# Performance work log

Measured on AMD Instinct MI355X. Metric: run time of the kernel, lower is better.

## Reference

```python
import jax, jax.numpy as jnp
import numpy as np

B, T, N, IN_DIM, H, C, L, S, P = 64, 13, 325, 2, 64, 4, 2, 4, 12
NC = S * N  # combined temporal-graph node count per batch element


def _make_adj(rng, n, density=0.03):
    mask = rng.random((n, n)) < density
    return (mask * rng.random((n, n))).astype(np.float32)


def _combine(adj, s, forward):
    n = adj.shape[0]
    out = np.zeros((n * s, n * s), np.float32)
    for i in range(s):
        out[i * n:(i + 1) * n, i * n:(i + 1) * n] = adj
        if forward and i < s - 1:
            out[i * n:(i + 1) * n, (i + 1) * n:(i + 2) * n] = np.eye(n, dtype=np.float32)
    return out


def _checkpoints(s, t):
    mark, cp = s, []
    while mark < t:
        cp.append(mark)
        mark += s - 1
    if cp[-1] != t:
        cp.append(t)
    return cp


def setup_inputs():
    key = jax.random.key(0)
    ks = jax.random.split(key, 20)
    rng = np.random.default_rng(0)
    adj = _make_adj(rng, N)
    pea = _make_adj(rng, N)
    sc = 0.05
    inp = {
        'inputs': jax.random.normal(ks[0], (B, T, N, IN_DIM), jnp.float32),
        'adj_fwd': jnp.asarray(_combine(adj, S, True)),
        'adj_bwd': jnp.asarray(_combine(adj, S, False)),
        'pea_fwd': jnp.asarray(_combine(pea, S, True)),
        'pea_bwd': jnp.asarray(_combine(pea, S, False)),
        'w_in': sc * jax.random.normal(ks[1], (IN_DIM, H), jnp.float32),
        'b_in': jnp.zeros((H,), jnp.float32),
        'res_w': sc * jax.random.normal(ks[2], (S,), jnp.float32),
        'res_b': jnp.zeros((), jnp.float32),
        'gconv_w': sc * jax.random.normal(ks[3], (S,), jnp.float32),
        'gconv_b': jnp.zeros((), jnp.float32),
        'gate1_w': sc * jax.random.normal(ks[4], (H, H), jnp.float32),
        'gate1_b': jnp.zeros((H,), jnp.float32),
        'gate2_w': sc * jax.random.normal(ks[5], (H, H * C), jnp.float32),
        'gate2_b': jnp.zeros((H * C,), jnp.float32),
        'reduce_w': sc * jax.random.normal(ks[6], (C * H, H), jnp.float32),
        'reduce_b': jnp.zeros((H,), jnp.float32),
        'gcn_adj_w': sc * jax.random.normal(ks[7], (C, L, 2, H, H), jnp.float32),
        'gcn_adj_b': jnp.zeros((C, L, H), jnp.float32),
        'gcn_pea_w': sc * jax.random.normal(ks[8], (C, L, 2, H, H), jnp.float32),
        'gcn_pea_b': jnp.zeros((C, L, H), jnp.float32),
        'out_conv_w': sc * jax.random.normal(ks[9], (P,), jnp.float32),
        'out_conv_b': jnp.zeros((P,), jnp.float32),
        'out_lin_w': sc * jax.random.normal(ks[10], (H, 1), jnp.float32),
        'out_lin_b': jnp.zeros((1,), jnp.float32),
    }
    return inp


def _gcn_stack(feats, W, b, A_f, A_b, n_out):
    # feats [B, S*N, H]; W [L, 2, H, H]; weighted message passing over both supports
    h = feats
    for l in range(W.shape[0]):
        mf = jnp.einsum('nm,bmh->bnh', A_f, h)
        mb = jnp.einsum('nm,bmh->bnh', A_b, h)
        h = jax.nn.relu(mf @ W[l, 0] + mb @ W[l, 1] + b[l])
    return h[:, -n_out:, :]  # last snapshot's nodes -> [B, N, H]


def reference(inputs, adj_fwd, adj_bwd, pea_fwd, pea_bwd, w_in, b_in, res_w, res_b,
              gconv_w, gconv_b, gate1_w, gate1_b, gate2_w, gate2_b, reduce_w, reduce_b,
              gcn_adj_w, gcn_adj_b, gcn_pea_w, gcn_pea_b, out_conv_w, out_conv_b,
              out_lin_w, out_lin_b):
    b_, t_, n_, _ = inputs.shape
    h_ = w_in.shape[1]
    s_ = res_w.shape[0]
    c_ = gcn_adj_w.shape[0]
    x = inputs @ w_in + b_in  # [B, T, N, H]
    last = None
    left = 0
    for idx, right in enumerate(_checkpoints(s_, t_)):
        fs = x[:, left:right] if idx == 0 else jnp.concatenate([last, x[:, left:right]], axis=1)  # [B,S,N,H]
        gf = (jnp.einsum('s,bsnh->bnh', gconv_w, fs) + gconv_b).reshape(b_ * n_, h_)
        residual = jnp.einsum('s,bsnh->bnh', res_w, fs) + res_b  # [B,N,H]
        feats = fs.reshape(b_, s_ * n_, h_)
        ca = jnp.concatenate(
            [_gcn_stack(feats, gcn_adj_w[c], gcn_adj_b[c], adj_fwd, adj_bwd, n_) for c in range(c_)],
            axis=-1).reshape(b_ * n_, c_ * h_)
        cp = jnp.concatenate(
            [_gcn_stack(feats, gcn_pea_w[c], gcn_pea_b[c], pea_fwd, pea_bwd, n_) for c in range(c_)],
            axis=-1).reshape(b_ * n_, c_ * h_)
        gate = jax.nn.sigmoid(jax.nn.relu(gf @ gate1_w + gate1_b) @ gate2_w + gate2_b)
        gr = gate * ca + (1.0 - gate) * cp
        gr = (gr @ reduce_w + reduce_b).reshape(b_, n_, h_)
        cr = gr + residual
        # nn.LayerNorm([B, N, H], elementwise_affine=False): normalize over whole tensor
        mu = jnp.mean(cr)
        var = jnp.var(cr)
        last = ((cr - mu) * jax.lax.rsqrt(var + 1e-5))[:, None]  # [B,1,N,H]
        left = right
    # 1x1 conv 1->pred_len over channel dim, then linear H->1
    out = jax.nn.relu(out_conv_w.reshape(1, -1, 1, 1) * last + out_conv_b.reshape(1, -1, 1, 1))
    out = out @ out_lin_w + out_lin_b  # [B, pred_len, N, 1]
    return out
```

## Files before the change

### kernel.cpp

```cpp
#include <hip/hip_runtime.h>
#include <hip/hip_bf16.h>
#include <math.h>

#define B_    64
#define T_    13
#define N_    325
#define H_    64
#define C_    4
#define L_    2
#define S_    4
#define P_    12
#define KCP   4
#define M_    (B_*N_)
#define ADJLD 1300
#define NNZCAP 64
#define WPITCH 72
#define MTP   264
#define RTP   264
#define NBLK  1300
#define MIXG  1304

typedef short bfrag __attribute__((ext_vector_type(8)));
typedef float f32x4 __attribute__((ext_vector_type(4)));

__device__ __forceinline__ void fma4(float4& a, float s, float4 x) {
    a.x += s * x.x; a.y += s * x.y; a.z += s * x.z; a.w += s * x.w;
}
__device__ __forceinline__ ushort bf_rne(float f) {
    unsigned u = __float_as_uint(f);
    return (ushort)((u + 0x7fffu + ((u >> 16) & 1u)) >> 16);
}
__device__ __forceinline__ uint2 pack_bf4(float4 v) {
    unsigned a = __float_as_uint(v.x), b = __float_as_uint(v.y);
    unsigned c = __float_as_uint(v.z), d = __float_as_uint(v.w);
    a = (a + 0x7fffu + ((a >> 16) & 1u)) >> 16;
    b = (b + 0x7fffu + ((b >> 16) & 1u)) >> 16;
    c = (c + 0x7fffu + ((c >> 16) & 1u)) >> 16;
    d = (d + 0x7fffu + ((d >> 16) & 1u)) >> 16;
    return make_uint2(a | (b << 16), c | (d << 16));
}
__device__ __forceinline__ float4 unpack_bf4(uint2 p) {
    return make_float4(__uint_as_float(p.x << 16),
                       __uint_as_float(p.x & 0xffff0000u),
                       __uint_as_float(p.y << 16),
                       __uint_as_float(p.y & 0xffff0000u));
}

__global__ void k_setup(
    const float* __restrict__ adj_fwd, const float* __restrict__ pea_fwd,
    const float* __restrict__ gadj_w, const float* __restrict__ gpea_w,
    const float* __restrict__ reduce_w,
    const float* __restrict__ gate1_w, const float* __restrict__ gate2_w,
    int* __restrict__ cnt, int* __restrict__ cols, float* __restrict__ vals,
    ushort* __restrict__ WT,
    ushort* __restrict__ RT, ushort* __restrict__ W1T, ushort* __restrict__ W2T)
{
    int bid = blockIdx.x, t = threadIdx.x;
    if (bid < 163) {
        int lane = t & 63, w = t >> 6;
        int row = bid * 4 + w;
        if (row >= 2 * N_) return;
        int mat = (row >= N_) ? 1 : 0;
        int n   = row - mat * N_;
        const float* A = mat ? pea_fwd : adj_fwd;
        const float* rp = A + (size_t)n * ADJLD;
        int* cw   = cols + (size_t)row * NNZCAP;
        float* vw = vals + (size_t)row * NNZCAP;
        int c = 0;
        for (int c0 = 0; c0 < 384; c0 += 64) {
            int col = c0 + lane;
            float v = (col < N_) ? rp[col] : 0.f;
            unsigned long long mmask = __ballot(v != 0.f);
            int idx = c + __popcll(mmask & ((1ull << lane) - 1ull));
            if (v != 0.f && idx < NNZCAP) { cw[idx] = col; vw[idx] = v; }
            c += __popcll(mmask);
        }
        if (c + lane < NNZCAP) { cw[c + lane] = 0; vw[c + lane] = 0.f; }
        if (lane == 0) cnt[row] = (c < NNZCAP) ? c : NNZCAP;
    } else if (bid == 163) {
        for (int i = 0; i < 64; ++i) {
            int e = t + i * 256;
            int k = e >> 6, n = e & 63;
            RT[(size_t)n * RTP + k] = bf_rne(reduce_w[e]);
        }
    } else if (bid < 180) {
        int mat = bid - 164;
        int layer = mat >> 3, sm = mat & 7;
        int stack = sm >> 2, c = sm & 3;
        const float* w0 = (stack ? gpea_w : gadj_w) + (size_t)((c * L_ + layer) * 2) * 4096;
        const float* w1 = w0 + 4096;
        for (int i = 0; i < 16; ++i) {
            int e = t + i * 256;
            int k = e >> 6, n = e & 63;
            WT[((size_t)mat * 64 + n) * WPITCH + k] = bf_rne(w0[e] + w1[e]);
        }
    } else if (bid == 180) {
        for (int i = 0; i < 16; ++i) {
            int e = t + i * 256;
            int k = e >> 6, n = e & 63;
            W1T[(size_t)n * WPITCH + k] = bf_rne(gate1_w[e]);
        }
    } else {
        for (int i = 0; i < 64; ++i) {
            int e = t + i * 256;
            int k = e >> 8, n = e & 255;
            W2T[(size_t)n * WPITCH + k] = bf_rne(gate2_w[e]);
        }
    }
}

__device__ __forceinline__ void l1_block(
    int vb, int t, int tt,
    const int*   __restrict__ cnt,
    const int*   __restrict__ cols,
    const float* __restrict__ vals,
    const float* __restrict__ inp,
    const float* __restrict__ w_in, const float* __restrict__ b_in,
    const ushort* __restrict__ WT,
    const float* __restrict__ badj, const float* __restrict__ bpea,
    ushort* __restrict__ G1a, ushort* __restrict__ G1p,
    ushort* MaH, ushort* MpH)
{
    int lane = t & 63, w = t >> 6;
    int m0 = vb * 32;
    int q = lane >> 4, ml = lane & 15;
    int colg = w * 16 + ml;

    bfrag BF[8][2];
    #pragma unroll
    for (int mat = 0; mat < 8; ++mat)
        #pragma unroll
        for (int kc = 0; kc < 2; ++kc)
            BF[mat][kc] = *(const bfrag*)&WT[((size_t)mat * 64 + colg) * WPITCH + kc * 32 + q * 8];

    {
        int row_l  = lane & 7;
        int stackl = (lane >> 3) & 1;
        int part   = lane >> 4;
        int m = m0 + w * 8 + row_l;
        int b = m / N_;
        int n = m - b * N_;
        const float* ipb = inp + ((size_t)(b * T_ + tt) * N_) * 2;
        int rowidx = stackl * N_ + n;
        const int*   cp = cols + (size_t)rowidx * NNZCAP;
        const float* vp = vals + (size_t)rowidx * NNZCAP;
        int myc = cnt[rowidx];
        float s0 = 0.f, s1 = 0.f, sv = 0.f;
        int   cn = cp[part];
        float vn = vp[part];
        for (int j = part; j < myc; j += 4) {
            int   c = cn;
            float v = vn;
            cn = cp[j + 4];
            vn = vp[j + 4];
            float2 x = *(const float2*)&ipb[(size_t)c * 2];
            s0 += v * x.x; s1 += v * x.y; sv += v;
        }
        s0 += __shfl_xor(s0, 16); s1 += __shfl_xor(s1, 16); sv += __shfl_xor(sv, 16);
        s0 += __shfl_xor(s0, 32); s1 += __shfl_xor(s1, 32); sv += __shfl_xor(sv, 32);
        float wa = w_in[lane], wb = w_in[H_ + lane], bi = b_in[lane];
        #pragma unroll
        for (int r = 0; r < 8; ++r) {
            float a0 = __shfl(s0, r),     a1 = __shfl(s1, r),     av = __shfl(sv, r);
            float p0 = __shfl(s0, 8 + r), p1 = __shfl(s1, 8 + r), pv = __shfl(sv, 8 + r);
            MaH[(w * 8 + r) * WPITCH + lane] = bf_rne(a0 * wa + a1 * wb + av * bi);
            MpH[(w * 8 + r) * WPITCH + lane] = bf_rne(p0 * wa + p1 * wb + pv * bi);
        }
    }
    __syncthreads();

    #pragma unroll
    for (int sc = 0; sc < 8; ++sc) {
        int stack = sc >> 2, c = sc & 3;
        const ushort* Msrc = stack ? MpH : MaH;
        float bv = (stack ? bpea : badj)[c * L_ * H_ + colg];
        ushort* Gout = stack ? G1p : G1a;
        #pragma unroll
        for (int r = 0; r < 2; ++r) {
            bfrag A0 = *(const bfrag*)&Msrc[(16 * r + ml) * WPITCH + q * 8];
            bfrag A1 = *(const bfrag*)&Msrc[(16 * r + ml) * WPITCH + 32 + q * 8];
            f32x4 acc = {0.f, 0.f, 0.f, 0.f};
            acc = __builtin_amdgcn_mfma_f32_16x16x32_bf16(A0, BF[sc][0], acc, 0, 0, 0);
            acc = __builtin_amdgcn_mfma_f32_16x16x32_bf16(A1, BF[sc][1], acc, 0, 0, 0);
            #pragma unroll
            for (int j = 0; j < 4; ++j) {
                float v = acc[j] + bv;
                v = v > 0.f ? v : 0.f;
                Gout[(size_t)(m0 + 16 * r + q * 4 + j) * 256 + c * 64 + colg] = bf_rne(v);
            }
        }
    }
}

__global__ __launch_bounds__(256, 4) void k_layer1(
    const int*   __restrict__ cnt,
    const int*   __restrict__ cols,
    const float* __restrict__ vals,
    const float* __restrict__ inp,
    const float* __restrict__ w_in, const float* __restrict__ b_in,
    const ushort* __restrict__ WT,
    const float* __restrict__ badj, const float* __restrict__ bpea,
    ushort* __restrict__ G1a4, ushort* __restrict__ G1p4)
{
    __shared__ __align__(16) ushort MaH[32 * WPITCH];
    __shared__ __align__(16) ushort MpH[32 * WPITCH];
    int vb = (blockIdx.x & 7) * 82 + (blockIdx.x >> 3);
    if (vb >= 650) return;
    l1_block(vb, threadIdx.x, 3, cnt, cols, vals,
             inp, w_in, b_in, WT, badj, bpea, G1a4, G1p4, MaH, MpH);
}

__global__ __launch_bounds__(256, 4) void k_mix(
    const float* __restrict__ inp,
    const float* __restrict__ w_in, const float* __restrict__ b_in,
    const float* __restrict__ gconv_w, const float* __restrict__ gconv_b,
    const float* __restrict__ res_w,   const float* __restrict__ res_b,
    const float* __restrict__ cr_in, int it,
    const ushort* __restrict__ W1T, const float* __restrict__ b1,
    const ushort* __restrict__ W2T, const float* __restrict__ b2,
    const int*   __restrict__ cnt,
    const int*   __restrict__ cols,
    const float* __restrict__ vals,
    const ushort* __restrict__ G1a, const ushort* __restrict__ G1p,
    const ushort* __restrict__ WT,
    const float* __restrict__ badj, const float* __restrict__ bpea,
    const ushort* __restrict__ RT,
    const float* __restrict__ reduce_b,
    float* __restrict__ cr,
    const float* __restrict__ partials_in,
    float* __restrict__ partials,
    int tt_l1,
    ushort* __restrict__ G1a_wr, ushort* __restrict__ G1p_wr)
{
    __shared__ __align__(16) ushort MtA[16 * MTP];
    __shared__ __align__(16) ushort MtP[16 * MTP];
    __shared__ __align__(16) ushort Gf[16 * WPITCH];
    __shared__ __align__(16) ushort Gr[16 * WPITCH];
    __shared__ float RES[16 * 68];
    __shared__ float red[8];
    int t = threadIdx.x, lane = t & 63, w = t >> 6;

    if (blockIdx.x >= MIXG) {
        int lx = blockIdx.x - MIXG;
        int vb1 = (lx & 7) * 82 + (lx >> 3);
        if (vb1 >= 650) return;
        l1_block(vb1, t, tt_l1, cnt, cols, vals, inp, w_in, b_in,
                 WT, badj, bpea, G1a_wr, G1p_wr, (ushort*)MtA, (ushort*)MtP);
        return;
    }

    int vb = (blockIdx.x & 7) * 163 + (blockIdx.x >> 3);
    if (vb >= NBLK) return;
    int m0 = vb * 16;
    int q = lane >> 4, ml = lane & 15;
    int colg = w * 16 + ml;

    float mu = 0.f, rs = 0.f;
    if (it > 0) {
        float a = 0.f, b = 0.f;
        for (int i = t; i < NBLK; i += 256) { a += partials_in[i]; b += partials_in[NBLK + i]; }
        #pragma unroll
        for (int off = 32; off > 0; off >>= 1) {
            a += __shfl_xor(a, off);
            b += __shfl_xor(b, off);
        }
        if (lane == 0) { red[w] = a; red[4 + w] = b; }
        __syncthreads();
        a = red[0] + red[1] + red[2] + red[3];
        b = red[4] + red[5] + red[6] + red[7];
        const float inv = 1.f / (float)(M_ * H_);
        mu = a * inv;
        float var = b * inv - mu * mu;
        rs = rsqrtf(var + 1e-5f);
    }

    {
        float wa = w_in[lane], wb = w_in[H_ + lane], bi = b_in[lane];
        float gw0 = gconv_w[0], gw1 = gconv_w[1], gw2 = gconv_w[2], gw3 = gconv_w[3];
        float rw0 = res_w[0],   rw1 = res_w[1],   rw2 = res_w[2],   rw3 = res_w[3];
        float gb = gconv_b[0],  rb = res_b[0];
        int t1 = (it == 0) ? 1 : (3 * it + 1);
        for (int i = 0; i < 4; ++i) {
            int r = i * 4 + w;
            int m = m0 + r;
            int b = m / N_, n = m % N_;
            const float* ipb = inp + ((size_t)b * T_ * N_ + n) * 2;
            float v0;
            if (it > 0) v0 = (cr_in[(size_t)m * H_ + lane] - mu) * rs;
            else        v0 = ipb[0] * wa + ipb[1] * wb + bi;
            const float* ip1 = ipb + (size_t)t1 * N_ * 2;
            const float* ip2 = ip1 + (size_t)N_ * 2;
            const float* ip3 = ip2 + (size_t)N_ * 2;
            float v1 = ip1[0] * wa + ip1[1] * wb + bi;
            float v2 = ip2[0] * wa + ip2[1] * wb + bi;
            float v3 = ip3[0] * wa + ip3[1] * wb + bi;
            Gf[r * WPITCH + lane] = bf_rne(gb + gw0 * v0 + gw1 * v1 + gw2 * v2 + gw3 * v3);
            RES[r * 68 + lane]    = rb + rw0 * v0 + rw1 * v1 + rw2 * v2 + rw3 * v3;
        }
    }
    __syncthreads();

    {
        bfrag A0 = *(const bfrag*)&Gf[ml * WPITCH + q * 8];
        bfrag A1 = *(const bfrag*)&Gf[ml * WPITCH + 32 + q * 8];
        bfrag B0 = *(const bfrag*)&W1T[(size_t)colg * WPITCH + q * 8];
        bfrag B1 = *(const bfrag*)&W1T[(size_t)colg * WPITCH + 32 + q * 8];
        f32x4 acc = {0.f, 0.f, 0.f, 0.f};
        acc = __builtin_amdgcn_mfma_f32_16x16x32_bf16(A0, B0, acc, 0, 0, 0);
        acc = __builtin_amdgcn_mfma_f32_16x16x32_bf16(A1, B1, acc, 0, 0, 0);
        float bb = b1[colg];
        #pragma unroll
        for (int j = 0; j < 4; ++j) {
            float v = acc[j] + bb;
            v = v > 0.f ? v : 0.f;
            Gr[(q * 4 + j) * WPITCH + colg] = bf_rne(v);
        }
    }
    __syncthreads();

    f32x4 gsv[4];
    {
        bfrag A0 = *(const bfrag*)&Gr[ml * WPITCH + q * 8];
        bfrag A1 = *(const bfrag*)&Gr[ml * WPITCH + 32 + q * 8];
        #pragma unroll
        for (int c = 0; c < 4; ++c) {
            bfrag B0 = *(const bfrag*)&W2T[(size_t)(c * 64 + colg) * WPITCH + q * 8];
            bfrag B1 = *(const bfrag*)&W2T[(size_t)(c * 64 + colg) * WPITCH + 32 + q * 8];
            f32x4 acc = {0.f, 0.f, 0.f, 0.f};
            acc = __builtin_amdgcn_mfma_f32_16x16x32_bf16(A0, B0, acc, 0, 0, 0);
            acc = __builtin_amdgcn_mfma_f32_16x16x32_bf16(A1, B1, acc, 0, 0, 0);
            float bb = b2[c * 64 + colg];
            #pragma unroll
            for (int j = 0; j < 4; ++j)
                gsv[c][j] = 1.f / (1.f + expf(-(acc[j] + bb)));
        }
    }

    for (int pp = 0; pp < 4; pp += 2) {
        int ma = m0 + w * 4 + pp, mb = ma + 1;
        int na = ma % N_, nb = mb % N_;
        const ushort* ga = G1a + (size_t)(ma - na) * 256 + lane * 4;
        const ushort* gb = G1a + (size_t)(mb - nb) * 256 + lane * 4;
        const ushort* pa = G1p + (size_t)(ma - na) * 256 + lane * 4;
        const ushort* pb = G1p + (size_t)(mb - nb) * 256 + lane * 4;
        const int   *cA0 = cols + na * NNZCAP,        *cB0 = cols + nb * NNZCAP;
        const float *vA0 = vals + na * NNZCAP,        *vB0 = vals + nb * NNZCAP;
        const int   *cA1 = cols + (N_ + na) * NNZCAP, *cB1 = cols + (N_ + nb) * NNZCAP;
        const float *vA1 = vals + (N_ + na) * NNZCAP, *vB1 = vals + (N_ + nb) * NNZCAP;
        int jm = max(max(cnt[na], cnt[nb]), max(cnt[N_ + na], cnt[N_ + nb]));
        float4 a0 = make_float4(0.f,0.f,0.f,0.f), a1 = make_float4(0.f,0.f,0.f,0.f);
        float4 p0 = make_float4(0.f,0.f,0.f,0.f), p1 = make_float4(0.f,0.f,0.f,0.f);
        int   nA00 = cA0[0], nA01 = cA0[1], nB00 = cB0[0], nB01 = cB0[1];
        int   nA10 = cA1[0], nA11 = cA1[1], nB10 = cB1[0], nB11 = cB1[1];
        float mA00 = vA0[0], mA01 = vA0[1], mB00 = vB0[0], mB01 = vB0[1];
        float mA10 = vA1[0], mA11 = vA1[1], mB10 = vB1[0], mB11 = vB1[1];
        for (int j = 0; j < jm; j += 2) {
            int   iA00 = nA00, iA01 = nA01, iB00 = nB00, iB01 = nB01;
            int   iA10 = nA10, iA11 = nA11, iB10 = nB10, iB11 = nB11;
            float uA00 = mA00, uA01 = mA01, uB00 = mB00, uB01 = mB01;
            float uA10 = mA10, uA11 = mA11, uB10 = mB10, uB11 = mB11;
            nA00 = cA0[j+2]; nA01 = cA0[j+3]; nB00 = cB0[j+2]; nB01 = cB0[j+3];
            nA10 = cA1[j+2]; nA11 = cA1[j+3]; nB10 = cB1[j+2]; nB11 = cB1[j+3];
            mA00 = vA0[j+2]; mA01 = vA0[j+3]; mB00 = vB0[j+2]; mB01 = vB0[j+3];
            mA10 = vA1[j+2]; mA11 = vA1[j+3]; mB10 = vB1[j+2]; mB11 = vB1[j+3];
            fma4(a0, uA00, unpack_bf4(*(const uint2*)&ga[iA00 * 256]));
            fma4(a0, uA01, unpack_bf4(*(const uint2*)&ga[iA01 * 256]));
            fma4(a1, uB00, unpack_bf4(*(const uint2*)&gb[iB00 * 256]));
            fma4(a1, uB01, unpack_bf4(*(const uint2*)&gb[iB01 * 256]));
            fma4(p0, uA10, unpack_bf4(*(const uint2*)&pa[iA10 * 256]));
            fma4(p0, uA11, unpack_bf4(*(const uint2*)&pa[iA11 * 256]));
            fma4(p1, uB10, unpack_bf4(*(const uint2*)&pb[iB10 * 256]));
            fma4(p1, uB11, unpack_bf4(*(const uint2*)&pb[iB11 * 256]));
        }
        int row0 = w * 4 + pp;
        *(uint2*)&MtA[row0 * MTP + lane * 4]       = pack_bf4(a0);
        *(uint2*)&MtA[(row0 + 1) * MTP + lane * 4] = pack_bf4(a1);
        *(uint2*)&MtP[row0 * MTP + lane * 4]       = pack_bf4(p0);
        *(uint2*)&MtP[(row0 + 1) * MTP + lane * 4] = pack_bf4(p1);
    }
    __syncthreads();

    const ushort* WT1 = WT + (size_t)8 * 64 * WPITCH;
    f32x4 res[4];
    bfrag B0c = *(const bfrag*)&WT1[(size_t)colg * WPITCH + q * 8];
    bfrag B1c = *(const bfrag*)&WT1[(size_t)colg * WPITCH + 32 + q * 8];
    #pragma unroll
    for (int sc = 0; sc < 8; ++sc) {
        int stack = sc >> 2, c = sc & 3;
        bfrag B0n = B0c, B1n = B1c;
        if (sc < 7) {
            B0n = *(const bfrag*)&WT1[((size_t)(sc + 1) * 64 + colg) * WPITCH + q * 8];
            B1n = *(const bfrag*)&WT1[((size_t)(sc + 1) * 64 + colg) * WPITCH + 32 + q * 8];
        }
        const ushort* Msrc = stack ? MtP : MtA;
        float bv = (stack ? bpea : badj)[(c * L_ + 1) * H_ + colg];
        bfrag A0 = *(const bfrag*)&Msrc[ml * MTP + c * 64 + q * 8];
        bfrag A1 = *(const bfrag*)&Msrc[ml * MTP + c * 64 + 32 + q * 8];
        f32x4 acc = {0.f, 0.f, 0.f, 0.f};
        acc = __builtin_amdgcn_mfma_f32_16x16x32_bf16(A0, B0c, acc, 0, 0, 0);
        acc = __builtin_amdgcn_mfma_f32_16x16x32_bf16(A1, B1c, acc, 0, 0, 0);
        #pragma unroll
        for (int j = 0; j < 4; ++j) {
            float v = acc[j] + bv;
            v = v > 0.f ? v : 0.f;
            if (stack == 0) res[c][j] = gsv[c][j] * v;
            else            res[c][j] += (1.f - gsv[c][j]) * v;
        }
        B0c = B0n; B1c = B1n;
    }

    bfrag RF[8];
    #pragma unroll
    for (int kc = 0; kc < 8; ++kc)
        RF[kc] = *(const bfrag*)&RT[(size_t)colg * RTP + kc * 32 + q * 8];
    f32x4 rv;
    #pragma unroll
    for (int j = 0; j < 4; ++j)
        rv[j] = RES[(q * 4 + j) * 68 + colg];

    __syncthreads();
    #pragma unroll
    for (int c = 0; c < 4; ++c)
        #pragma unroll
        for (int j = 0; j < 4; ++j)
            MtA[(q * 4 + j) * MTP + c * 64 + colg] = bf_rne(res[c][j]);
    __syncthreads();

    f32x4 racc = {0.f, 0.f, 0.f, 0.f};
    #pragma unroll
    for (int kc = 0; kc < 8; ++kc) {
        bfrag A0 = *(const bfrag*)&MtA[ml * MTP + kc * 32 + q * 8];
        racc = __builtin_amdgcn_mfma_f32_16x16x32_bf16(A0, RF[kc], racc, 0, 0, 0);
    }

    float bi = reduce_b[colg];
    float s = 0.f, s2 = 0.f;
    #pragma unroll
    for (int j = 0; j < 4; ++j) {
        int m = m0 + q * 4 + j;
        float v = racc[j] + bi + rv[j];
        cr[(size_t)m * 64 + colg] = v;
        s += v; s2 += v * v;
    }
    #pragma unroll
    for (int off = 32; off > 0; off >>= 1) {
        s  += __shfl_xor(s, off);
        s2 += __shfl_xor(s2, off);
    }
    if (lane == 0) { red[w] = s; red[4 + w] = s2; }
    __syncthreads();
    if (t == 0) partials[vb]        = red[0] + red[1] + red[2] + red[3];
    if (t == 1) partials[NBLK + vb] = red[4] + red[5] + red[6] + red[7];
}

__global__ __launch_bounds__(64) void k_out(
    const float* __restrict__ cr, const float* __restrict__ partials,
    const float* __restrict__ ocw, const float* __restrict__ ocb,
    const float* __restrict__ olw, const float* __restrict__ olb,
    float* __restrict__ out) {
    int t = threadIdx.x;
    float a = 0.f, b2s = 0.f;
    for (int i = t; i < NBLK; i += 64) { a += partials[i]; b2s += partials[NBLK + i]; }
    #pragma unroll
    for (int off = 32; off > 0; off >>= 1) {
        a   += __shfl_xor(a, off);
        b2s += __shfl_xor(b2s, off);
    }
    const float inv = 1.f / (float)(M_ * H_);
    float mu  = a * inv;
    float var = b2s * inv - mu * mu;
    float rs  = rsqrtf(var + 1e-5f);

    int m = blockIdx.x * 64 + t;
    int b = m / N_, n = m % N_;
    float cw[P_], cb[P_], acc[P_];
    #pragma unroll
    for (int p = 0; p < P_; ++p) { cw[p] = ocw[p]; cb[p] = ocb[p]; acc[p] = 0.f; }
    const float* lr = cr + (size_t)m * H_;
    for (int h4 = 0; h4 < 64; h4 += 4) {
        float4 lv4 = *(const float4*)&lr[h4];
        float4 wv4 = *(const float4*)&olw[h4];
        float lv[4] = {(lv4.x - mu) * rs, (lv4.y - mu) * rs,
                       (lv4.z - mu) * rs, (lv4.w - mu) * rs};
        float wv[4] = {wv4.x, wv4.y, wv4.z, wv4.w};
        #pragma unroll
        for (int e = 0; e < 4; ++e) {
            float lvv = lv[e], wvv = wv[e];
            #pragma unroll
            for (int p = 0; p < P_; ++p) {
                float u = cw[p] * lvv + cb[p];
                u = u > 0.f ? u : 0.f;
                acc[p] += u * wvv;
            }
        }
    }
    float ob = olb[0];
    #pragma unroll
    for (int p = 0; p < P_; ++p)
        out[(size_t)(b * P_ + p) * N_ + n] = acc[p] + ob;
}

extern "C" void kernel_launch(void* const* d_in, const int* in_sizes, int n_in,
                              void* d_out, int out_size, void* d_ws, size_t ws_size,
                              hipStream_t stream) {
    const float* inp      = (const float*)d_in[0];
    const float* adj_fwd  = (const float*)d_in[1];
    const float* pea_fwd  = (const float*)d_in[3];
    const float* w_in     = (const float*)d_in[5];
    const float* b_in     = (const float*)d_in[6];
    const float* res_w    = (const float*)d_in[7];
    const float* res_b    = (const float*)d_in[8];
    const float* gconv_w  = (const float*)d_in[9];
    const float* gconv_b  = (const float*)d_in[10];
    const float* gate1_w  = (const float*)d_in[11];
    const float* gate1_b  = (const float*)d_in[12];
    const float* gate2_w  = (const float*)d_in[13];
    const float* gate2_b  = (const float*)d_in[14];
    const float* reduce_w = (const float*)d_in[15];
    const float* reduce_b = (const float*)d_in[16];
    const float* gadj_w   = (const float*)d_in[17];
    const float* gadj_b   = (const float*)d_in[18];
    const float* gpea_w   = (const float*)d_in[19];
    const float* gpea_b   = (const float*)d_in[20];
    const float* ocw      = (const float*)d_in[21];
    const float* ocb      = (const float*)d_in[22];
    const float* olw      = (const float*)d_in[23];
    const float* olb      = (const float*)d_in[24];
    float* out = (float*)d_out;

    float* ws       = (float*)d_ws;
    float* cr       = ws;
    float* partials = cr + (size_t)M_ * H_;
    int*   scnt  = (int*)(partials + 2 * NBLK);
    int*   scols = scnt + 2 * N_;
    float* svals = (float*)(scols + 2 * N_ * NNZCAP);
    ushort* G1a4 = (ushort*)(svals + 2 * N_ * NNZCAP);
    ushort* G1p4 = G1a4 + 2 * (size_t)M_ * 256;
    ushort* WT   = G1p4 + 2 * (size_t)M_ * 256;
    WT = (ushort*)(((uintptr_t)WT + 15) & ~(uintptr_t)15);
    ushort* RT   = WT + 16 * 64 * WPITCH;
    ushort* W1T  = RT + 64 * RTP;
    ushort* W2T  = W1T + 64 * WPITCH;

    k_setup<<<182, 256, 0, stream>>>(
        adj_fwd, pea_fwd, gadj_w, gpea_w, reduce_w,
        gate1_w, gate2_w, scnt, scols, svals, WT, RT, W1T, W2T);

    k_layer1<<<656, 256, 0, stream>>>(
        scnt, scols, svals, inp, w_in, b_in, WT, gadj_b, gpea_b, G1a4, G1p4);

    for (int it = 0; it < 4; ++it) {
        int slot = it & 1;
        int embed = (it < 3);
        int grid  = MIXG + (embed ? 656 : 0);
        int wrsl  = (it + 1) & 1;
        k_mix<<<grid, 256, 0, stream>>>(
            inp, w_in, b_in, gconv_w, gconv_b, res_w, res_b, cr, it,
            W1T, gate1_b, W2T, gate2_b,
            scnt, scols, svals,
            G1a4 + (size_t)slot * M_ * 256, G1p4 + (size_t)slot * M_ * 256,
            WT, gadj_b, gpea_b, RT, reduce_b, cr, partials, partials,
            3 * (it + 1) + 3,
            G1a4 + (size_t)wrsl * M_ * 256, G1p4 + (size_t)wrsl * M_ * 256);
    }

    k_out<<<N_, 64, 0, stream>>>(cr, partials, ocw, ocb, olw, olb, out);
}
```

Before: 402.1 us.

## Fuse all stages into one cooperative persistent kernel with grid syncs

Replaces the chain of setup, layer-1, four mix launches and output launch with a single cooperative kernel that loops over the stages persistently and separates them with grid-wide barriers. Partial statistics are double-buffered so one stage's LayerNorm partials are not overwritten while they are still being read. The aim is to remove kernel launch gaps and tail effects between the roughly seven dependent launches. The cost is grid.sync overhead and a grid capped by occupancy, so blocks loop over the work. The original multi-launch path is kept as a fallback if the cooperative launch fails.

```diff
diff --git a/kernel.cpp b/kernel.cpp
--- a/kernel.cpp
+++ b/kernel.cpp
@@ -1,6 +1,9 @@
 #include <hip/hip_runtime.h>
 #include <hip/hip_bf16.h>
+#include <hip/hip_cooperative_groups.h>
 #include <math.h>
+
+namespace cg = cooperative_groups;
 
 #define B_    64
 #define T_    13
@@ -10,7 +13,6 @@
 #define L_    2
 #define S_    4
 #define P_    12
-#define KCP   4
 #define M_    (B_*N_)
 #define ADJLD 1300
 #define NNZCAP 64
@@ -46,26 +48,29 @@
                        __uint_as_float(p.y & 0xffff0000u));
 }
 
-__global__ void k_setup(
-    const float* __restrict__ adj_fwd, const float* __restrict__ pea_fwd,
-    const float* __restrict__ gadj_w, const float* __restrict__ gpea_w,
-    const float* __restrict__ reduce_w,
-    const float* __restrict__ gate1_w, const float* __restrict__ gate2_w,
-    int* __restrict__ cnt, int* __restrict__ cols, float* __restrict__ vals,
-    ushort* __restrict__ WT,
-    ushort* __restrict__ RT, ushort* __restrict__ W1T, ushort* __restrict__ W2T)
-{
-    int bid = blockIdx.x, t = threadIdx.x;
+struct MP {
+    const float *inp, *adj_fwd, *pea_fwd;
+    const float *w_in, *b_in, *res_w, *res_b, *gconv_w, *gconv_b;
+    const float *gate1_w, *gate1_b, *gate2_w, *gate2_b;
+    const float *reduce_w, *reduce_b;
+    const float *gadj_w, *gadj_b, *gpea_w, *gpea_b;
+    const float *ocw, *ocb, *olw, *olb;
+    int *scnt; int *scols; float *svals;
+    ushort *G1a4, *G1p4, *WT, *RT, *W1T, *W2T;
+    float *cr, *pb0, *pb1, *out;
+};
+
+__device__ __forceinline__ void do_setup(int bid, int t, const MP& p) {
     if (bid < 163) {
         int lane = t & 63, w = t >> 6;
         int row = bid * 4 + w;
         if (row >= 2 * N_) return;
         int mat = (row >= N_) ? 1 : 0;
         int n   = row - mat * N_;
-        const float* A = mat ? pea_fwd : adj_fwd;
+        const float* A = mat ? p.pea_fwd : p.adj_fwd;
         const float* rp = A + (size_t)n * ADJLD;
-        int* cw   = cols + (size_t)row * NNZCAP;
-        float* vw = vals + (size_t)row * NNZCAP;
+        int* cw   = p.scols + (size_t)row * NNZCAP;
+        float* vw = p.svals + (size_t)row * NNZCAP;
         int c = 0;
         for (int c0 = 0; c0 < 384; c0 += 64) {
             int col = c0 + lane;
@@ -76,48 +81,41 @@
             c += __popcll(mmask);
         }
         if (c + lane < NNZCAP) { cw[c + lane] = 0; vw[c + lane] = 0.f; }
-        if (lane == 0) cnt[row] = (c < NNZCAP) ? c : NNZCAP;
+        if (lane == 0) p.scnt[row] = (c < NNZCAP) ? c : NNZCAP;
     } else if (bid == 163) {
         for (int i = 0; i < 64; ++i) {
             int e = t + i * 256;
             int k = e >> 6, n = e & 63;
-            RT[(size_t)n * RTP + k] = bf_rne(reduce_w[e]);
+            p.RT[(size_t)n * RTP + k] = bf_rne(p.reduce_w[e]);
         }
     } else if (bid < 180) {
         int mat = bid - 164;
         int layer = mat >> 3, sm = mat & 7;
         int stack = sm >> 2, c = sm & 3;
-        const float* w0 = (stack ? gpea_w : gadj_w) + (size_t)((c * L_ + layer) * 2) * 4096;
+        const float* w0 = (stack ? p.gpea_w : p.gadj_w) + (size_t)((c * L_ + layer) * 2) * 4096;
         const float* w1 = w0 + 4096;
         for (int i = 0; i < 16; ++i) {
             int e = t + i * 256;
             int k = e >> 6, n = e & 63;
-            WT[((size_t)mat * 64 + n) * WPITCH + k] = bf_rne(w0[e] + w1[e]);
+            p.WT[((size_t)mat * 64 + n) * WPITCH + k] = bf_rne(w0[e] + w1[e]);
         }
     } else if (bid == 180) {
         for (int i = 0; i < 16; ++i) {
             int e = t + i * 256;
             int k = e >> 6, n = e & 63;
-            W1T[(size_t)n * WPITCH + k] = bf_rne(gate1_w[e]);
-        }
-    } else {
+            p.W1T[(size_t)n * WPITCH + k] = bf_rne(p.gate1_w[e]);
+        }
+    } else if (bid == 181) {
         for (int i = 0; i < 64; ++i) {
             int e = t + i * 256;
             int k = e >> 8, n = e & 255;
-            W2T[(size_t)n * WPITCH + k] = bf_rne(gate2_w[e]);
+            p.W2T[(size_t)n * WPITCH + k] = bf_rne(p.gate2_w[e]);
         }
     }
 }
 
 __device__ __forceinline__ void l1_block(
-    int vb, int t, int tt,
-    const int*   __restrict__ cnt,
-    const int*   __restrict__ cols,
-    const float* __restrict__ vals,
-    const float* __restrict__ inp,
-    const float* __restrict__ w_in, const float* __restrict__ b_in,
-    const ushort* __restrict__ WT,
-    const float* __restrict__ badj, const float* __restrict__ bpea,
+    int vb, int t, int tt, const MP& p,
     ushort* __restrict__ G1a, ushort* __restrict__ G1p,
     ushort* MaH, ushort* MpH)
 {
@@ -131,7 +129,7 @@
     for (int mat = 0; mat < 8; ++mat)
         #pragma unroll
         for (int kc = 0; kc < 2; ++kc)
-            BF[mat][kc] = *(const bfrag*)&WT[((size_t)mat * 64 + colg) * WPITCH + kc * 32 + q * 8];
+            BF[mat][kc] = *(const bfrag*)&p.WT[((size_t)mat * 64 + colg) * WPITCH + kc * 32 + q * 8];
 
     {
         int row_l  = lane & 7;
@@ -140,11 +138,11 @@
         int m = m0 + w * 8 + row_l;
         int b = m / N_;
         int n = m - b * N_;
-        const float* ipb = inp + ((size_t)(b * T_ + tt) * N_) * 2;
+        const float* ipb = p.inp + ((size_t)(b * T_ + tt) * N_) * 2;
         int rowidx = stackl * N_ + n;
-        const int*   cp = cols + (size_t)rowidx * NNZCAP;
-        const float* vp = vals + (size_t)rowidx * NNZCAP;
-        int myc = cnt[rowidx];
+        const int*   cp = p.scols + (size_t)rowidx * NNZCAP;
+        const float* vp = p.svals + (size_t)rowidx * NNZCAP;
+        int myc = p.scnt[rowidx];
         float s0 = 0.f, s1 = 0.f, sv = 0.f;
         int   cn = cp[part];
         float vn = vp[part];
@@ -158,7 +156,7 @@
         }
         s0 += __shfl_xor(s0, 16); s1 += __shfl_xor(s1, 16); sv += __shfl_xor(sv, 16);
         s0 += __shfl_xor(s0, 32); s1 += __shfl_xor(s1, 32); sv += __shfl_xor(sv, 32);
-        float wa = w_in[lane], wb = w_in[H_ + lane], bi = b_in[lane];
+        float wa = p.w_in[lane], wb = p.w_in[H_ + lane], bi = p.b_in[lane];
         #pragma unroll
         for (int r = 0; r < 8; ++r) {
             float a0 = __shfl(s0, r),     a1 = __shfl(s1, r),     av = __shfl(sv, r);
@@ -173,7 +171,7 @@
     for (int sc = 0; sc < 8; ++sc) {
         int stack = sc >> 2, c = sc & 3;
         const ushort* Msrc = stack ? MpH : MaH;
-        float bv = (stack ? bpea : badj)[c * L_ * H_ + colg];
+        float bv = (stack ? p.gpea_b : p.gadj_b)[c * L_ * H_ + colg];
         ushort* Gout = stack ? G1p : G1a;
         #pragma unroll
         for (int r = 0; r < 2; ++r) {
@@ -192,65 +190,13 @@
     }
 }
 
-__global__ __launch_bounds__(256, 4) void k_layer1(
-    const int*   __restrict__ cnt,
-    const int*   __restrict__ cols,
-    const float* __restrict__ vals,
-    const float* __restrict__ inp,
-    const float* __restrict__ w_in, const float* __restrict__ b_in,
-    const ushort* __restrict__ WT,
-    const float* __restrict__ badj, const float* __restrict__ bpea,
-    ushort* __restrict__ G1a4, ushort* __restrict__ G1p4)
+__device__ __forceinline__ void mix_block(
+    int vb, int t, int it, const MP& p,
+    const ushort* __restrict__ G1a, const ushort* __restrict__ G1p,
+    const float* __restrict__ pin, float* __restrict__ pout,
+    ushort* MtA, ushort* MtP, ushort* Gf, ushort* Gr, float* RES, float* red)
 {
-    __shared__ __align__(16) ushort MaH[32 * WPITCH];
-    __shared__ __align__(16) ushort MpH[32 * WPITCH];
-    int vb = (blockIdx.x & 7) * 82 + (blockIdx.x >> 3);
-    if (vb >= 650) return;
-    l1_block(vb, threadIdx.x, 3, cnt, cols, vals,
-             inp, w_in, b_in, WT, badj, bpea, G1a4, G1p4, MaH, MpH);
-}
-
-__global__ __launch_bounds__(256, 4) void k_mix(
-    const float* __restrict__ inp,
-    const float* __restrict__ w_in, const float* __restrict__ b_in,
-    const float* __restrict__ gconv_w, const float* __restrict__ gconv_b,
-    const float* __restrict__ res_w,   const float* __restrict__ res_b,
-    const float* __restrict__ cr_in, int it,
-    const ushort* __restrict__ W1T, const float* __restrict__ b1,
-    const ushort* __restrict__ W2T, const float* __restrict__ b2,
-    const int*   __restrict__ cnt,
-    const int*   __restrict__ cols,
-    const float* __restrict__ vals,
-    const ushort* __restrict__ G1a, const ushort* __restrict__ G1p,
-    const ushort* __restrict__ WT,
-    const float* __restrict__ badj, const float* __restrict__ bpea,
-    const ushort* __restrict__ RT,
-    const float* __restrict__ reduce_b,
-    float* __restrict__ cr,
-    const float* __restrict__ partials_in,
-    float* __restrict__ partials,
-    int tt_l1,
-    ushort* __restrict__ G1a_wr, ushort* __restrict__ G1p_wr)
-{
-    __shared__ __align__(16) ushort MtA[16 * MTP];
-    __shared__ __align__(16) ushort MtP[16 * MTP];
-    __shared__ __align__(16) ushort Gf[16 * WPITCH];
-    __shared__ __align__(16) ushort Gr[16 * WPITCH];
-    __shared__ float RES[16 * 68];
-    __shared__ float red[8];
-    int t = threadIdx.x, lane = t & 63, w = t >> 6;
-
-    if (blockIdx.x >= MIXG) {
-        int lx = blockIdx.x - MIXG;
-        int vb1 = (lx & 7) * 82 + (lx >> 3);
-        if (vb1 >= 650) return;
-        l1_block(vb1, t, tt_l1, cnt, cols, vals, inp, w_in, b_in,
-                 WT, badj, bpea, G1a_wr, G1p_wr, (ushort*)MtA, (ushort*)MtP);
-        return;
-    }
-
-    int vb = (blockIdx.x & 7) * 163 + (blockIdx.x >> 3);
-    if (vb >= NBLK) return;
+    int lane = t & 63, w = t >> 6;
     int m0 = vb * 16;
     int q = lane >> 4, ml = lane & 15;
     int colg = w * 16 + ml;
@@ -258,7 +204,7 @@
     float mu = 0.f, rs = 0.f;
     if (it > 0) {
         float a = 0.f, b = 0.f;
-        for (int i = t; i < NBLK; i += 256) { a += partials_in[i]; b += partials_in[NBLK + i]; }
+        for (int i = t; i < NBLK; i += 256) { a += pin[i]; b += pin[NBLK + i]; }
         #pragma unroll
         for (int off = 32; off > 0; off >>= 1) {
             a += __shfl_xor(a, off);
@@ -275,18 +221,18 @@
     }
 
     {
-        float wa = w_in[lane], wb = w_in[H_ + lane], bi = b_in[lane];
-        float gw0 = gconv_w[0], gw1 = gconv_w[1], gw2 = gconv_w[2], gw3 = gconv_w[3];
-        float rw0 = res_w[0],   rw1 = res_w[1],   rw2 = res_w[2],   rw3 = res_w[3];
-        float gb = gconv_b[0],  rb = res_b[0];
+        float wa = p.w_in[lane], wb = p.w_in[H_ + lane], bi = p.b_in[lane];
+        float gw0 = p.gconv_w[0], gw1 = p.gconv_w[1], gw2 = p.gconv_w[2], gw3 = p.gconv_w[3];
+        float rw0 = p.res_w[0],   rw1 = p.res_w[1],   rw2 = p.res_w[2],   rw3 = p.res_w[3];
+        float gb = p.gconv_b[0],  rb = p.res_b[0];
         int t1 = (it == 0) ? 1 : (3 * it + 1);
         for (int i = 0; i < 4; ++i) {
             int r = i * 4 + w;
             int m = m0 + r;
             int b = m / N_, n = m % N_;
-            const float* ipb = inp + ((size_t)b * T_ * N_ + n) * 2;
+            const float* ipb = p.inp + ((size_t)b * T_ * N_ + n) * 2;
             float v0;
-            if (it > 0) v0 = (cr_in[(size_t)m * H_ + lane] - mu) * rs;
+            if (it > 0) v0 = (p.cr[(size_t)m * H_ + lane] - mu) * rs;
             else        v0 = ipb[0] * wa + ipb[1] * wb + bi;
             const float* ip1 = ipb + (size_t)t1 * N_ * 2;
             const float* ip2 = ip1 + (size_t)N_ * 2;
@@ -303,12 +249,12 @@
     {
         bfrag A0 = *(const bfrag*)&Gf[ml * WPITCH + q * 8];
         bfrag A1 = *(const bfrag*)&Gf[ml * WPITCH + 32 + q * 8];
-        bfrag B0 = *(const bfrag*)&W1T[(size_t)colg * WPITCH + q * 8];
-        bfrag B1 = *(const bfrag*)&W1T[(size_t)colg * WPITCH + 32 + q * 8];
+        bfrag B0 = *(const bfrag*)&p.W1T[(size_t)colg * WPITCH + q * 8];
+        bfrag B1 = *(const bfrag*)&p.W1T[(size_t)colg * WPITCH + 32 + q * 8];
         f32x4 acc = {0.f, 0.f, 0.f, 0.f};
         acc = __builtin_amdgcn_mfma_f32_16x16x32_bf16(A0, B0, acc, 0, 0, 0);
         acc = __builtin_amdgcn_mfma_f32_16x16x32_bf16(A1, B1, acc, 0, 0, 0);
-        float bb = b1[colg];
+        float bb = p.gate1_b[colg];
         #pragma unroll
         for (int j = 0; j < 4; ++j) {
             float v = acc[j] + bb;
@@ -324,12 +270,12 @@
         bfrag A1 = *(const bfrag*)&Gr[ml * WPITCH + 32 + q * 8];
         #pragma unroll
         for (int c = 0; c < 4; ++c) {
-            bfrag B0 = *(const bfrag*)&W2T[(size_t)(c * 64 + colg) * WPITCH + q * 8];
-            bfrag B1 = *(const bfrag*)&W2T[(size_t)(c * 64 + colg) * WPITCH + 32 + q * 8];
+            bfrag B0 = *(const bfrag*)&p.W2T[(size_t)(c * 64 + colg) * WPITCH + q * 8];
+            bfrag B1 = *(const bfrag*)&p.W2T[(size_t)(c * 64 + colg) * WPITCH + 32 + q * 8];
             f32x4 acc = {0.f, 0.f, 0.f, 0.f};
             acc = __builtin_amdgcn_mfma_f32_16x16x32_bf16(A0, B0, acc, 0, 0, 0);
             acc = __builtin_amdgcn_mfma_f32_16x16x32_bf16(A1, B1, acc, 0, 0, 0);
-            float bb = b2[c * 64 + colg];
+            float bb = p.gate2_b[c * 64 + colg];
             #pragma unroll
             for (int j = 0; j < 4; ++j)
                 gsv[c][j] = 1.f / (1.f + expf(-(acc[j] + bb)));
@@ -343,11 +289,11 @@
         const ushort* gb = G1a + (size_t)(mb - nb) * 256 + lane * 4;
         const ushort* pa = G1p + (size_t)(ma - na) * 256 + lane * 4;
         const ushort* pb = G1p + (size_t)(mb - nb) * 256 + lane * 4;
-        const int   *cA0 = cols + na * NNZCAP,        *cB0 = cols + nb * NNZCAP;
-        const float *vA0 = vals + na * NNZCAP,        *vB0 = vals + nb * NNZCAP;
-        const int   *cA1 = cols + (N_ + na) * NNZCAP, *cB1 = cols + (N_ + nb) * NNZCAP;
-        const float *vA1 = vals + (N_ + na) * NNZCAP, *vB1 = vals + (N_ + nb) * NNZCAP;
-        int jm = max(max(cnt[na], cnt[nb]), max(cnt[N_ + na], cnt[N_ + nb]));
+        const int   *cA0 = p.scols + na * NNZCAP,        *cB0 = p.scols + nb * NNZCAP;
+        const float *vA0 = p.svals + na * NNZCAP,        *vB0 = p.svals + nb * NNZCAP;
+        const int   *cA1 = p.scols + (N_ + na) * NNZCAP, *cB1 = p.scols + (N_ + nb) * NNZCAP;
+        const float *vA1 = p.svals + (N_ + na) * NNZCAP, *vB1 = p.svals + (N_ + nb) * NNZCAP;
+        int jm = max(max(p.scnt[na], p.scnt[nb]), max(p.scnt[N_ + na], p.scnt[N_ + nb]));
         float4 a0 = make_float4(0.f,0.f,0.f,0.f), a1 = make_float4(0.f,0.f,0.f,0.f);
         float4 p0 = make_float4(0.f,0.f,0.f,0.f), p1 = make_float4(0.f,0.f,0.f,0.f);
         int   nA00 = cA0[0], nA01 = cA0[1], nB00 = cB0[0], nB01 = cB0[1];
@@ -380,7 +326,7 @@
     }
     __syncthreads();
 
-    const ushort* WT1 = WT + (size_t)8 * 64 * WPITCH;
+    const ushort* WT1 = p.WT + (size_t)8 * 64 * WPITCH;
     f32x4 res[4];
     bfrag B0c = *(const bfrag*)&WT1[(size_t)colg * WPITCH + q * 8];
     bfrag B1c = *(const bfrag*)&WT1[(size_t)colg * WPITCH + 32 + q * 8];
@@ -393,7 +339,7 @@
             B1n = *(const bfrag*)&WT1[((size_t)(sc + 1) * 64 + colg) * WPITCH + 32 + q * 8];
         }
         const ushort* Msrc = stack ? MtP : MtA;
-        float bv = (stack ? bpea : badj)[(c * L_ + 1) * H_ + colg];
+        float bv = (stack ? p.gpea_b : p.gadj_b)[(c * L_ + 1) * H_ + colg];
         bfrag A0 = *(const bfrag*)&Msrc[ml * MTP + c * 64 + q * 8];
         bfrag A1 = *(const bfrag*)&Msrc[ml * MTP + c * 64 + 32 + q * 8];
         f32x4 acc = {0.f, 0.f, 0.f, 0.f};
@@ -412,7 +358,7 @@
     bfrag RF[8];
     #pragma unroll
     for (int kc = 0; kc < 8; ++kc)
-        RF[kc] = *(const bfrag*)&RT[(size_t)colg * RTP + kc * 32 + q * 8];
+        RF[kc] = *(const bfrag*)&p.RT[(size_t)colg * RTP + kc * 32 + q * 8];
     f32x4 rv;
     #pragma unroll
     for (int j = 0; j < 4; ++j)
@@ -433,13 +379,13 @@
         racc = __builtin_amdgcn_mfma_f32_16x16x32_bf16(A0, RF[kc], racc, 0, 0, 0);
     }
 
-    float bi = reduce_b[colg];
+    float bi = p.reduce_b[colg];
     float s = 0.f, s2 = 0.f;
     #pragma unroll
     for (int j = 0; j < 4; ++j) {
         int m = m0 + q * 4 + j;
         float v = racc[j] + bi + rv[j];
-        cr[(size_t)m * 64 + colg] = v;
+        p.cr[(size_t)m * 64 + colg] = v;
         s += v; s2 += v * v;
     }
     #pragma unroll
@@ -449,37 +395,170 @@
     }
     if (lane == 0) { red[w] = s; red[4 + w] = s2; }
     __syncthreads();
-    if (t == 0) partials[vb]        = red[0] + red[1] + red[2] + red[3];
-    if (t == 1) partials[NBLK + vb] = red[4] + red[5] + red[6] + red[7];
-}
-
-__global__ __launch_bounds__(64) void k_out(
-    const float* __restrict__ cr, const float* __restrict__ partials,
-    const float* __restrict__ ocw, const float* __restrict__ ocb,
-    const float* __restrict__ olw, const float* __restrict__ olb,
-    float* __restrict__ out) {
-    int t = threadIdx.x;
+    if (t == 0) pout[vb]        = red[0] + red[1] + red[2] + red[3];
+    if (t == 1) pout[NBLK + vb] = red[4] + red[5] + red[6] + red[7];
+}
+
+__device__ __forceinline__ void do_out(int bid, int t, const MP& p,
+                                       const float* __restrict__ pbuf, float* red)
+{
+    int lane = t & 63, w = t >> 6;
     float a = 0.f, b2s = 0.f;
-    for (int i = t; i < NBLK; i += 64) { a += partials[i]; b2s += partials[NBLK + i]; }
+    for (int i = t; i < NBLK; i += 256) { a += pbuf[i]; b2s += pbuf[NBLK + i]; }
     #pragma unroll
     for (int off = 32; off > 0; off >>= 1) {
         a   += __shfl_xor(a, off);
         b2s += __shfl_xor(b2s, off);
     }
+    if (lane == 0) { red[w] = a; red[4 + w] = b2s; }
+    __syncthreads();
+    a   = red[0] + red[1] + red[2] + red[3];
+    b2s = red[4] + red[5] + red[6] + red[7];
     const float inv = 1.f / (float)(M_ * H_);
     float mu  = a * inv;
     float var = b2s * inv - mu * mu;
     float rs  = rsqrtf(var + 1e-5f);
 
+    int m = bid * 256 + t;
+    if (m >= M_) return;
+    int b = m / N_, n = m % N_;
+    float cw[P_], cb[P_], acc[P_];
+    #pragma unroll
+    for (int pp = 0; pp < P_; ++pp) { cw[pp] = p.ocw[pp]; cb[pp] = p.ocb[pp]; acc[pp] = 0.f; }
+    const float* lr = p.cr + (size_t)m * H_;
+    for (int h4 = 0; h4 < 64; h4 += 4) {
+        float4 lv4 = *(const float4*)&lr[h4];
+        float4 wv4 = *(const float4*)&p.olw[h4];
+        float lv[4] = {(lv4.x - mu) * rs, (lv4.y - mu) * rs,
+                       (lv4.z - mu) * rs, (lv4.w - mu) * rs};
+        float wv[4] = {wv4.x, wv4.y, wv4.z, wv4.w};
+        #pragma unroll
+        for (int e = 0; e < 4; ++e) {
+            float lvv = lv[e], wvv = wv[e];
+            #pragma unroll
+            for (int pp = 0; pp < P_; ++pp) {
+                float u = cw[pp] * lvv + cb[pp];
+                u = u > 0.f ? u : 0.f;
+                acc[pp] += u * wvv;
+            }
+        }
+    }
+    float ob = p.olb[0];
+    #pragma unroll
+    for (int pp = 0; pp < P_; ++pp)
+        p.out[(size_t)(b * P_ + pp) * N_ + n] = acc[pp] + ob;
+}
+
+__global__ __launch_bounds__(256, 4) void k_mega(MP p)
+{
+    __shared__ __align__(16) ushort MtA[16 * MTP];
+    __shared__ __align__(16) ushort MtP[16 * MTP];
+    __shared__ __align__(16) ushort Gf[16 * WPITCH];
+    __shared__ __align__(16) ushort Gr[16 * WPITCH];
+    __shared__ float RES[16 * 68];
+    __shared__ float red[8];
+    cg::grid_group grid = cg::this_grid();
+    int bid = blockIdx.x, t = threadIdx.x, G = gridDim.x;
+
+    if (bid < 182) do_setup(bid, t, p);
+    grid.sync();
+
+    for (int v = bid; v < 656; v += G) {
+        int vb = (v & 7) * 82 + (v >> 3);
+        if (vb < 650)
+            l1_block(vb, t, 3, p, p.G1a4, p.G1p4, (ushort*)MtA, (ushort*)MtP);
+        __syncthreads();
+    }
+    grid.sync();
+
+    for (int it = 0; it < 4; ++it) {
+        const float* pin  = (it & 1) ? p.pb0 : p.pb1;
+        float*       pout = (it & 1) ? p.pb1 : p.pb0;
+        const ushort* G1a_rd = p.G1a4 + (size_t)(it & 1) * M_ * 256;
+        const ushort* G1p_rd = p.G1p4 + (size_t)(it & 1) * M_ * 256;
+        ushort* G1a_wr = p.G1a4 + (size_t)((it + 1) & 1) * M_ * 256;
+        ushort* G1p_wr = p.G1p4 + (size_t)((it + 1) & 1) * M_ * 256;
+        int nv  = (it < 3) ? (MIXG + 656) : MIXG;
+        int tt1 = 3 * (it + 1) + 3;
+        for (int v = bid; v < nv; v += G) {
+            if (v < MIXG) {
+                int vb = (v & 7) * 163 + (v >> 3);
+                if (vb < NBLK)
+                    mix_block(vb, t, it, p, G1a_rd, G1p_rd, pin, pout,
+                              MtA, MtP, Gf, Gr, RES, red);
+            } else {
+                int lx = v - MIXG;
+                int vb1 = (lx & 7) * 82 + (lx >> 3);
+                if (vb1 < 650)
+                    l1_block(vb1, t, tt1, p, G1a_wr, G1p_wr, (ushort*)MtA, (ushort*)MtP);
+            }
+            __syncthreads();
+        }
+        grid.sync();
+    }
+
+    if (bid * 256 < M_) do_out(bid, t, p, p.pb1, red);
+}
+
+__global__ void k_setup(MP p) { do_setup(blockIdx.x, threadIdx.x, p); }
+
+__global__ __launch_bounds__(256, 4) void k_layer1(MP p) {
+    __shared__ __align__(16) ushort MaH[32 * WPITCH];
+    __shared__ __align__(16) ushort MpH[32 * WPITCH];
+    int vb = (blockIdx.x & 7) * 82 + (blockIdx.x >> 3);
+    if (vb >= 650) return;
+    l1_block(vb, threadIdx.x, 3, p, p.G1a4, p.G1p4, MaH, MpH);
+}
+
+__global__ __launch_bounds__(256, 4) void k_mix(MP p, int it) {
+    __shared__ __align__(16) ushort MtA[16 * MTP];
+    __shared__ __align__(16) ushort MtP[16 * MTP];
+    __shared__ __align__(16) ushort Gf[16 * WPITCH];
+    __shared__ __align__(16) ushort Gr[16 * WPITCH];
+    __shared__ float RES[16 * 68];
+    __shared__ float red[8];
+    int t = threadIdx.x;
+    if (blockIdx.x >= MIXG) {
+        int lx = blockIdx.x - MIXG;
+        int vb1 = (lx & 7) * 82 + (lx >> 3);
+        if (vb1 >= 650) return;
+        l1_block(vb1, t, 3 * (it + 1) + 3, p,
+                 p.G1a4 + (size_t)((it + 1) & 1) * M_ * 256,
+                 p.G1p4 + (size_t)((it + 1) & 1) * M_ * 256,
+                 (ushort*)MtA, (ushort*)MtP);
+        return;
+    }
+    int vb = (blockIdx.x & 7) * 163 + (blockIdx.x >> 3);
+    if (vb >= NBLK) return;
+    mix_block(vb, t, it, p,
+              p.G1a4 + (size_t)(it & 1) * M_ * 256,
+              p.G1p4 + (size_t)(it & 1) * M_ * 256,
+              p.pb0, p.pb0, MtA, MtP, Gf, Gr, RES, red);
+}
+
+__global__ __launch_bounds__(64) void k_out(MP p) {
+    int t = threadIdx.x;
+    float a = 0.f, b2s = 0.f;
+    for (int i = t; i < NBLK; i += 64) { a += p.pb0[i]; b2s += p.pb0[NBLK + i]; }
+    #pragma unroll
+    for (int off = 32; off > 0; off >>= 1) {
+        a   += __shfl_xor(a, off);
+        b2s += __shfl_xor(b2s, off);
+    }
+    const float inv = 1.f / (float)(M_ * H_);
+    float mu  = a * inv;
+    float var = b2s * inv - mu * mu;
+    float rs  = rsqrtf(var + 1e-5f);
+
     int m = blockIdx.x * 64 + t;
     int b = m / N_, n = m % N_;
     float cw[P_], cb[P_], acc[P_];
     #pragma unroll
-    for (int p = 0; p < P_; ++p) { cw[p] = ocw[p]; cb[p] = ocb[p]; acc[p] = 0.f; }
-    const float* lr = cr + (size_t)m * H_;
+    for (int pp = 0; pp < P_; ++pp) { cw[pp] = p.ocw[pp]; cb[pp] = p.ocb[pp]; acc[pp] = 0.f; }
+    const float* lr = p.cr + (size_t)m * H_;
     for (int h4 = 0; h4 < 64; h4 += 4) {
         float4 lv4 = *(const float4*)&lr[h4];
-        float4 wv4 = *(const float4*)&olw[h4];
+        float4 wv4 = *(const float4*)&p.olw[h4];
         float lv[4] = {(lv4.x - mu) * rs, (lv4.y - mu) * rs,
                        (lv4.z - mu) * rs, (lv4.w - mu) * rs};
         float wv[4] = {wv4.x, wv4.y, wv4.z, wv4.w};
@@ -487,82 +566,80 @@
         for (int e = 0; e < 4; ++e) {
             float lvv = lv[e], wvv = wv[e];
             #pragma unroll
-            for (int p = 0; p < P_; ++p) {
-                float u = cw[p] * lvv + cb[p];
+            for (int pp = 0; pp < P_; ++pp) {
+                float u = cw[pp] * lvv + cb[pp];
                 u = u > 0.f ? u : 0.f;
-                acc[p] += u * wvv;
+                acc[pp] += u * wvv;
             }
         }
     }
-    float ob = olb[0];
-    #pragma unroll
-    for (int p = 0; p < P_; ++p)
-        out[(size_t)(b * P_ + p) * N_ + n] = acc[p] + ob;
+    float ob = p.olb[0];
+    #pragma unroll
+    for (int pp = 0; pp < P_; ++pp)
+        p.out[(size_t)(b * P_ + pp) * N_ + n] = acc[pp] + ob;
 }
 
 extern "C" void kernel_launch(void* const* d_in, const int* in_sizes, int n_in,
                               void* d_out, int out_size, void* d_ws, size_t ws_size,
                               hipStream_t stream) {
-    const float* inp      = (const float*)d_in[0];
-    const float* adj_fwd  = (const float*)d_in[1];
-    const float* pea_fwd  = (const float*)d_in[3];
-    const float* w_in     = (const float*)d_in[5];
-    const float* b_in     = (const float*)d_in[6];
-    const float* res_w    = (const float*)d_in[7];
-    const float* res_b    = (const float*)d_in[8];
-    const float* gconv_w  = (const float*)d_in[9];
-    const float* gconv_b  = (const float*)d_in[10];
-    const float* gate1_w  = (const float*)d_in[11];
-    const float* gate1_b  = (const float*)d_in[12];
-    const float* gate2_w  = (const float*)d_in[13];
-    const float* gate2_b  = (const float*)d_in[14];
-    const float* reduce_w = (const float*)d_in[15];
-    const float* reduce_b = (const float*)d_in[16];
-    const float* gadj_w   = (const float*)d_in[17];
-    const float* gadj_b   = (const float*)d_in[18];
-    const float* gpea_w   = (const float*)d_in[19];
-    const float* gpea_b   = (const float*)d_in[20];
-    const float* ocw      = (const float*)d_in[21];
-    const float* ocb      = (const float*)d_in[22];
-    const float* olw      = (const float*)d_in[23];
-    const float* olb      = (const float*)d_in[24];
-    float* out = (float*)d_out;
-
-    float* ws       = (float*)d_ws;
-    float* cr       = ws;
-    float* partials = cr + (size_t)M_ * H_;
-    int*   scnt  = (int*)(partials + 2 * NBLK);
-    int*   scols = scnt + 2 * N_;
-    float* svals = (float*)(scols + 2 * N_ * NNZCAP);
-    ushort* G1a4 = (ushort*)(svals + 2 * N_ * NNZCAP);
-    ushort* G1p4 = G1a4 + 2 * (size_t)M_ * 256;
-    ushort* WT   = G1p4 + 2 * (size_t)M_ * 256;
+    MP p;
+    p.inp      = (const float*)d_in[0];
+    p.adj_fwd  = (const float*)d_in[1];
+    p.pea_fwd  = (const float*)d_in[3];
+    p.w_in     = (const float*)d_in[5];
+    p.b_in     = (const float*)d_in[6];
+    p.res_w    = (const float*)d_in[7];
+    p.res_b    = (const float*)d_in[8];
+    p.gconv_w  = (const float*)d_in[9];
+    p.gconv_b  = (const float*)d_in[10];
+    p.gate1_w  = (const float*)d_in[11];
+    p.gate1_b  = (const float*)d_in[12];
+    p.gate2_w  = (const float*)d_in[13];
+    p.gate2_b  = (const float*)d_in[14];
+    p.reduce_w = (const float*)d_in[15];
+    p.reduce_b = (const float*)d_in[16];
+    p.gadj_w   = (const float*)d_in[17];
+    p.gadj_b   = (const float*)d_in[18];
+    p.gpea_w   = (const float*)d_in[19];
+    p.gpea_b   = (const float*)d_in[20];
+    p.ocw      = (const float*)d_in[21];
+    p.ocb      = (const float*)d_in[22];
+    p.olw      = (const float*)d_in[23];
+    p.olb      = (const float*)d_in[24];
+    p.out      = (float*)d_out;
+
+    float* ws = (float*)d_ws;
+    p.cr   = ws;
+    p.pb0  = p.cr + (size_t)M_ * H_;
+    p.pb1  = p.pb0 + 2 * NBLK;
+    p.scnt = (int*)(p.pb1 + 2 * NBLK);
+    p.scols = p.scnt + 2 * N_;
+    p.svals = (float*)(p.scols + 2 * N_ * NNZCAP);
+    p.G1a4 = (ushort*)(p.svals + 2 * N_ * NNZCAP);
+    p.G1p4 = p.G1a4 + 2 * (size_t)M_ * 256;
+    ushort* WT = p.G1p4 + 2 * (size_t)M_ * 256;
     WT = (ushort*)(((uintptr_t)WT + 15) & ~(uintptr_t)15);
-    ushort* RT   = WT + 16 * 64 * WPITCH;
-    ushort* W1T  = RT + 64 * RTP;
-    ushort* W2T  = W1T + 64 * WPITCH;
-
-    k_setup<<<182, 256, 0, stream>>>(
-        adj_fwd, pea_fwd, gadj_w, gpea_w, reduce_w,
-        gate1_w, gate2_w, scnt, scols, svals, WT, RT, W1T, W2T);
-
-    k_layer1<<<656, 256, 0, stream>>>(
-        scnt, scols, svals, inp, w_in, b_in, WT, gadj_b, gpea_b, G1a4, G1p4);
-
-    for (int it = 0; it < 4; ++it) {
-        int slot = it & 1;
-        int embed = (it < 3);
-        int grid  = MIXG + (embed ? 656 : 0);
-        int wrsl  = (it + 1) & 1;
-        k_mix<<<grid, 256, 0, stream>>>(
-            inp, w_in, b_in, gconv_w, gconv_b, res_w, res_b, cr, it,
-            W1T, gate1_b, W2T, gate2_b,
-            scnt, scols, svals,
-            G1a4 + (size_t)slot * M_ * 256, G1p4 + (size_t)slot * M_ * 256,
-            WT, gadj_b, gpea_b, RT, reduce_b, cr, partials, partials,
-            3 * (it + 1) + 3,
-            G1a4 + (size_t)wrsl * M_ * 256, G1p4 + (size_t)wrsl * M_ * 256);
-    }
-
-    k_out<<<N_, 64, 0, stream>>>(cr, partials, ocw, ocb, olw, olb, out);
-}
+    p.WT  = WT;
+    p.RT  = WT + 16 * 64 * WPITCH;
+    p.W1T = p.RT + 64 * RTP;
+    p.W2T = p.W1T + 64 * WPITCH;
+
+    int occ = 0;
+    hipError_t oe = hipOccupancyMaxActiveBlocksPerMultiprocessor(&occ, k_mega, 256, 0);
+    hipError_t le = hipErrorUnknown;
+    if (oe == hipSuccess && occ >= 1) {
+        int grid = occ * 256;
+        if (grid > MIXG + 656) grid = MIXG + 656;
+        void* args[] = { (void*)&p };
+        le = hipLaunchCooperativeKernel(k_mega, dim3(grid), dim3(256), args, 0u, stream);
+    }
+    if (le != hipSuccess) {
+        k_setup<<<182, 256, 0, stream>>>(p);
+        k_layer1<<<656, 256, 0, stream>>>(p);
+        for (int it = 0; it < 4; ++it) {
+            int grid = MIXG + ((it < 3) ? 656 : 0);
+            k_mix<<<grid, 256, 0, stream>>>(p, it);
+        }
+        k_out<<<N_, 64, 0, stream>>>(p);
+    }
+}
```

Measured after the change: 1.182 ms. 194% more time.
